# Kernel tuning notes

Hardware: AMD Instinct MI355X
Metric: run time of the kernel (lower is better)

Reference implementation:

```python
import jax, jax.numpy as jnp
import numpy as np

DIM = 128
DIM_HEAD = 32
HEADS = DIM // DIM_HEAD
WS = 7  # window_size
N = WS ** 3  # tokens per window = 343
TABLE = (2 * WS - 1) ** 3  # 2197


def _rel_pos_indices():
    pos = np.arange(WS)
    grid = np.stack(np.meshgrid(pos, pos, pos, indexing='ij'))  # [3,WS,WS,WS]
    grid = grid.reshape(3, -1).T  # [N,3]
    rel = grid[:, None, :] - grid[None, :, :] + (WS - 1)  # [N,N,3]
    idx = (rel * np.array([(2 * WS - 1) ** 2, 2 * WS - 1, 1])).sum(-1)
    return jnp.asarray(idx, jnp.int32)  # [N,N]


def setup_inputs() -> dict:
    key = jax.random.key(0)
    k1, k2, k3, k4 = jax.random.split(key, 4)
    x = jax.random.normal(k1, (2, 4, 4, 4, WS, WS, WS, DIM), dtype=jnp.float32)
    ln_w = jnp.ones((DIM,), jnp.float32)
    ln_b = jnp.zeros((DIM,), jnp.float32)
    w_qkv = jax.random.normal(k2, (DIM, 3 * DIM), jnp.float32) * 0.02
    w_out = jax.random.normal(k3, (DIM, DIM), jnp.float32) * 0.02
    bias_table = jax.random.normal(k4, (TABLE, HEADS), jnp.float32) * 0.02
    return {"x": x, "ln_w": ln_w, "ln_b": ln_b, "w_qkv": w_qkv,
            "w_out": w_out, "bias_table": bias_table,
            "rel_pos_indices": _rel_pos_indices()}


def reference(x, ln_w, ln_b, w_qkv, w_out, bias_table, rel_pos_indices):
    b, H, W, F, wh, ww, wf, d = x.shape
    scale = DIM_HEAD ** -0.5
    # LayerNorm over last dim (eps=1e-5, torch default)
    mu = x.mean(-1, keepdims=True)
    var = ((x - mu) ** 2).mean(-1, keepdims=True)
    xn = (x - mu) * jax.lax.rsqrt(var + 1e-5) * ln_w + ln_b
    # merge windows: [(b H W F), N, d]
    xr = xn.reshape(-1, wh * ww * wf, d)
    qkv = xr @ w_qkv  # [B, N, 3d]
    q, k, v = jnp.split(qkv, 3, axis=-1)
    def heads(t):
        B, n, _ = t.shape
        return t.reshape(B, n, HEADS, DIM_HEAD).transpose(0, 2, 1, 3)  # [B,h,N,dh]
    q, k, v = heads(q) * scale, heads(k), heads(v)
    sim = jnp.einsum('bhid,bhjd->bhij', q, k)  # [B,h,N,N]
    bias = bias_table[rel_pos_indices]  # [N,N,h]
    sim = sim + bias.transpose(2, 0, 1)[None]  # add [1,h,N,N]
    attn = jax.nn.softmax(sim, axis=-1)
    out = jnp.einsum('bhij,bhjd->bhid', attn, v)  # [B,h,N,dh]
    out = out.transpose(0, 2, 1, 3).reshape(-1, wh * ww * wf, d)
    out = out @ w_out
    return out.reshape(b, H, W, F, wh, ww, wf, d)
```

## Files before the change

### kernel.cpp

```cpp
#include <hip/hip_runtime.h>
#include <cstddef>
#include <cstdint>


#define NTOK 343
#define NPAD 352
#define NT   22
#define LOG2E 1.4426950408889634f
#define QSCALE (0.17677669529663687f * 1.4426950408889634f)

typedef short short8 __attribute__((ext_vector_type(8)));
typedef float f32x4  __attribute__((ext_vector_type(4)));

__device__ __forceinline__ unsigned short f2b(float f) {
    unsigned int u = __float_as_uint(f);
    u = (u + 0x7FFFu + ((u >> 16) & 1u)) >> 16;
    return (unsigned short)u;
}
__device__ __forceinline__ unsigned pk_bf16(float a, float b) {
    unsigned r;
    asm("v_cvt_pk_bf16_f32 %0, %1, %2" : "=v"(r) : "v"(a), "v"(b));
    return r;
}
__device__ __forceinline__ float fast_exp2(float x) {
#if __has_builtin(__builtin_amdgcn_exp2f)
    return __builtin_amdgcn_exp2f(x);
#else
    return exp2f(x);
#endif
}
__device__ __forceinline__ float blo(unsigned u){ return __uint_as_float(u << 16); }
__device__ __forceinline__ float bhi(unsigned u){ return __uint_as_float(u & 0xffff0000u); }

__global__ __launch_bounds__(256) void prep_weights(
    const float* __restrict__ wqkv, const float* __restrict__ wout,
    unsigned short* __restrict__ wqT_sw, unsigned short* __restrict__ woT)
{
    int t = blockIdx.x * 256 + threadIdx.x;
    if (t < 49152) {
        int s = t >> 14, within = t & 16383;
        int r = within & 127, k = within >> 7;
        float f = wqkv[k * 384 + s * 128 + r];
        if (s == 0) f *= QSCALE;
        wqT_sw[s * 16384 + ((r * 128 + k) ^ ((r & 7) << 3))] = f2b(f);
    } else {
        int t2 = t - 49152;
        int n = t2 & 127, k = t2 >> 7;
        woT[n * 128 + k] = f2b(wout[k * 128 + n]);
    }
}

__global__ __launch_bounds__(256) void prep_bias(
    const float* __restrict__ table, const int* __restrict__ rel,
    unsigned short* __restrict__ biasb)
{
    int t = blockIdx.x * 256 + threadIdx.x;
    int r  = t & 3;
    int tp = (t >> 2) & 1;
    int i  = (t >> 3) % NPAD;
    int rest = (t >> 3) / NPAD;
    int g  = rest & 3;  rest >>= 2;
    int c  = rest % 11;
    int h  = rest / 11;
    int j  = (2 * c + tp) * 16 + g * 4 + r;
    float v;
    if (j >= NTOK)      v = -1e30f;
    else if (i >= NTOK) v = 0.0f;
    else                v = table[rel[i * NTOK + j] * 4 + h] * LOG2E;
    biasb[t] = f2b(v);
}

__global__ __launch_bounds__(256) void ln_x(
    const float* __restrict__ x, const float* __restrict__ lnw, const float* __restrict__ lnb,
    unsigned short* __restrict__ xnsw)
{
    const int by = blockIdx.x, t = threadIdx.x;
    const int r = t >> 1, hf = t & 1;
    const size_t row = (size_t)by * 128 + r;
    const float* src = x + row * 128 + hf * 64;
    char* dst = reinterpret_cast<char*>(xnsw) + (size_t)by * 32768;
    float vals[64];
    float s = 0.f, s2 = 0.f;
    #pragma unroll
    for (int c = 0; c < 16; ++c) {
        float4 v = *reinterpret_cast<const float4*>(src + c * 4);
        vals[c*4+0] = v.x; vals[c*4+1] = v.y; vals[c*4+2] = v.z; vals[c*4+3] = v.w;
        s  += v.x + v.y + v.z + v.w;
        s2 += v.x*v.x + v.y*v.y + v.z*v.z + v.w*v.w;
    }
    s  += __shfl_xor(s, 1, 64);
    s2 += __shfl_xor(s2, 1, 64);
    const float mu   = s * (1.f / 128.f);
    const float var  = s2 * (1.f / 128.f) - mu * mu;
    const float rstd = rsqrtf(var + 1e-5f);
    #pragma unroll
    for (int c = 0; c < 8; ++c) {
        unsigned int packed[4];
        #pragma unroll
        for (int e = 0; e < 4; ++e) {
            int idx = c * 8 + e * 2;
            int col = hf * 64 + idx;
            float a = (vals[idx]   - mu) * rstd * lnw[col]   + lnb[col];
            float b = (vals[idx+1] - mu) * rstd * lnw[col+1] + lnb[col+1];
            packed[e] = pk_bf16(a, b);
        }
        int off = (r * 256 + hf * 128 + c * 16) ^ ((r & 7) << 4);
        *reinterpret_cast<int4*>(dst + off) = *reinterpret_cast<const int4*>(packed);
    }
}

__global__ __launch_bounds__(256) void qkv_gemm(
    const unsigned short* __restrict__ xnsw, const unsigned short* __restrict__ wqT_sw,
    unsigned short* __restrict__ qkv_rm)
{
    __shared__ __align__(16) char smem[65536];
    const int bx = blockIdx.x, by = blockIdx.y, t = threadIdx.x;

    {
        const char* srcA = reinterpret_cast<const char*>(xnsw) + (size_t)by * 32768;
        const char* srcB = reinterpret_cast<const char*>(wqT_sw) + (size_t)bx * 32768;
        #pragma unroll
        for (int p = 0; p < 8; ++p) {
            int off = p * 4096 + t * 16;
            *reinterpret_cast<int4*>(smem + off) = *reinterpret_cast<const int4*>(srcA + off);
            *reinterpret_cast<int4*>(smem + 32768 + off) = *reinterpret_cast<const int4*>(srcB + off);
        }
    }
    __syncthreads();

    const int lane = t & 63, wid = t >> 6;
    const int l15 = lane & 15, g = lane >> 4;
    const int wr = wid >> 1, wc = wid & 1;

    f32x4 acc[4][4] = {};
    #pragma unroll
    for (int ks = 0; ks < 4; ++ks) {
        short8 a[4], b[4];
        #pragma unroll
        for (int mt = 0; mt < 4; ++mt) {
            int row = wr * 64 + mt * 16 + l15;
            int off = (row * 256 + ks * 64 + g * 16) ^ ((row & 7) << 4);
            a[mt] = *reinterpret_cast<const short8*>(smem + off);
        }
        #pragma unroll
        for (int nt = 0; nt < 4; ++nt) {
            int row = wc * 64 + nt * 16 + l15;
            int off = (row * 256 + ks * 64 + g * 16) ^ ((row & 7) << 4);
            b[nt] = *reinterpret_cast<const short8*>(smem + 32768 + off);
        }
        #pragma unroll
        for (int mt = 0; mt < 4; ++mt)
            #pragma unroll
            for (int nt = 0; nt < 4; ++nt)
                acc[mt][nt] = __builtin_amdgcn_mfma_f32_16x16x32_bf16(a[mt], b[nt], acc[mt][nt], 0, 0, 0);
    }
    __syncthreads();

    #pragma unroll
    for (int mt = 0; mt < 4; ++mt) {
        #pragma unroll
        for (int nt = 0; nt < 4; ++nt) {
            unsigned w01 = pk_bf16(acc[mt][nt][0], acc[mt][nt][1]);
            unsigned w23 = pk_bf16(acc[mt][nt][2], acc[mt][nt][3]);
            int col = wc * 64 + nt * 16 + l15;
            int rb  = wr * 64 + mt * 16 + g * 4;
            unsigned short v4[4] = {(unsigned short)w01, (unsigned short)(w01 >> 16),
                                    (unsigned short)w23, (unsigned short)(w23 >> 16)};
            #pragma unroll
            for (int r4 = 0; r4 < 4; ++r4) {
                int row = rb + r4;
                int off = (row * 256 + col * 2) ^ ((row & 28) << 2);
                *reinterpret_cast<unsigned short*>(smem + off) = v4[r4];
            }
        }
    }
    __syncthreads();

    #pragma unroll
    for (int p = 0; p < 8; ++p) {
        int flat = p * 4096 + t * 16;
        int row = flat >> 8, cb = flat & 255;
        int off = (row * 256 + cb) ^ ((row & 28) << 2);
        int4 v = *reinterpret_cast<const int4*>(smem + off);
        unsigned token = (unsigned)(by * 128 + row);
        unsigned w = token / 343u;
        unsigned n = token - w * 343u;
        *reinterpret_cast<int4*>(qkv_rm + ((size_t)w * NPAD + n) * 384 + bx * 128 + (cb >> 1)) = v;
    }
}

__global__ __launch_bounds__(512, 4) void attn(
    const unsigned short* __restrict__ qkv_rm, const unsigned short* __restrict__ biasb,
    unsigned short* __restrict__ ao)
{
    __shared__ __align__(16) unsigned short klds[4 * NPAD * 8];
    __shared__ __align__(16) unsigned short vlds[44 * 272];
    __shared__ __align__(16) unsigned short pbuf[8][4][16][8];
    const int bw = blockIdx.x >> 2, h = blockIdx.x & 3;
    const int t = threadIdx.x, lane = t & 63, wid = t >> 6;
    const int l15 = lane & 15, g = lane >> 4;

    const unsigned short* base = qkv_rm + (size_t)bw * NPAD * 384;

    #pragma unroll
    for (int p = 0; p < 6; ++p) {
        int id = p * 512 + t;
        if (id < 2816) {
            bool isK = id < 1408;
            int id2 = isK ? id : id - 1408;
            int n = id2 >> 2, q4 = id2 & 3;
            const unsigned short* src = base + (size_t)n * 384 + (isK ? 128 : 256) + h * 32 + q4 * 8;
            int4 v = *reinterpret_cast<const int4*>(src);
            if (isK) {
                *reinterpret_cast<int4*>(&klds[(q4 * NPAD + n) * 8]) = v;
            } else {
                const unsigned short* sv = reinterpret_cast<const unsigned short*>(&v);
                int jb = n >> 3, e = n & 7;
                #pragma unroll
                for (int q = 0; q < 8; ++q)
                    vlds[jb * 272 + (q4 * 8 + q) * 8 + e] = sv[q];
            }
        }
    }
    __syncthreads();

    const f32x4 zero4 = {0.f, 0.f, 0.f, 0.f};
    for (int it = wid; it < NT; it += 8) {
        const int i = it * 16 + l15;
        short8 qf = *reinterpret_cast<const short8*>(base + (size_t)i * 384 + h * 32 + g * 8);
        short8 bb[11];
        #pragma unroll
        for (int c = 0; c < 11; ++c)
            bb[c] = *reinterpret_cast<const short8*>(biasb + (size_t)(((h * 11 + c) * 4 + g) * NPAD + i) * 8);

        float s = 0.f;
        f32x4 o0 = zero4, o1 = zero4;
        #pragma unroll
        for (int c = 0; c < 11; ++c) {
            short8 kf0 = *reinterpret_cast<const short8*>(&klds[(g * NPAD + 2 * c * 16 + l15) * 8]);
            short8 kf1 = *reinterpret_cast<const short8*>(&klds[(g * NPAD + (2 * c + 1) * 16 + l15) * 8]);
            f32x4 a0 = __builtin_amdgcn_mfma_f32_16x16x32_bf16(kf0, qf, zero4, 0, 0, 0);
            f32x4 a1 = __builtin_amdgcn_mfma_f32_16x16x32_bf16(kf1, qf, zero4, 0, 0, 0);
            const unsigned* bu = reinterpret_cast<const unsigned*>(&bb[c]);
            float p0 = fast_exp2(a0[0] + blo(bu[0]));
            float p1 = fast_exp2(a0[1] + bhi(bu[0]));
            float p2 = fast_exp2(a0[2] + blo(bu[1]));
            float p3 = fast_exp2(a0[3] + bhi(bu[1]));
            float p4 = fast_exp2(a1[0] + blo(bu[2]));
            float p5 = fast_exp2(a1[1] + bhi(bu[2]));
            float p6 = fast_exp2(a1[2] + blo(bu[3]));
            float p7 = fast_exp2(a1[3] + bhi(bu[3]));
            s += ((p0 + p1) + (p2 + p3)) + ((p4 + p5) + (p6 + p7));
            uint2 w0; w0.x = pk_bf16(p0, p1); w0.y = pk_bf16(p2, p3);
            uint2 w1; w1.x = pk_bf16(p4, p5); w1.y = pk_bf16(p6, p7);
            *reinterpret_cast<uint2*>(&pbuf[wid][(g >> 1)][l15][(g & 1) * 4]) = w0;
            *reinterpret_cast<uint2*>(&pbuf[wid][2 + (g >> 1)][l15][(g & 1) * 4]) = w1;
            short8 pf = *reinterpret_cast<const short8*>(&pbuf[wid][g][l15][0]);
            short8 vf0 = *reinterpret_cast<const short8*>(&vlds[(c * 4 + g) * 272 + l15 * 8]);
            short8 vf1 = *reinterpret_cast<const short8*>(&vlds[(c * 4 + g) * 272 + (16 + l15) * 8]);
            o0 = __builtin_amdgcn_mfma_f32_16x16x32_bf16(vf0, pf, o0, 0, 0, 0);
            o1 = __builtin_amdgcn_mfma_f32_16x16x32_bf16(vf1, pf, o1, 0, 0, 0);
        }
        s += __shfl_xor(s, 16, 64);
        s += __shfl_xor(s, 32, 64);
        const float rinv = 1.f / s;

        unsigned short* aorow = ao + ((size_t)bw * NPAD + i) * 128 + h * 32;
        uint2 q0; q0.x = pk_bf16(o0[0] * rinv, o0[1] * rinv); q0.y = pk_bf16(o0[2] * rinv, o0[3] * rinv);
        uint2 q1; q1.x = pk_bf16(o1[0] * rinv, o1[1] * rinv); q1.y = pk_bf16(o1[2] * rinv, o1[3] * rinv);
        *reinterpret_cast<uint2*>(aorow + g * 4) = q0;
        *reinterpret_cast<uint2*>(aorow + 16 + g * 4) = q1;
    }
}

__global__ __launch_bounds__(256) void outproj(
    const unsigned short* __restrict__ ao, const unsigned short* __restrict__ woT,
    float* __restrict__ out)
{
    __shared__ __align__(16) char smem[65536];
    const int t = threadIdx.x;
    const int m0 = blockIdx.x * 128;
    {
        const int r = t >> 1, hf = t & 1;
        const unsigned short* src = ao + (size_t)(m0 + r) * 128 + hf * 64;
        #pragma unroll
        for (int c = 0; c < 8; ++c) {
            int4 v = *reinterpret_cast<const int4*>(src + c * 8);
            int off = (r * 256 + hf * 128 + c * 16) ^ ((r & 7) << 4);
            *reinterpret_cast<int4*>(smem + off) = v;
        }
        const unsigned short* src2 = woT + (size_t)r * 128 + hf * 64;
        #pragma unroll
        for (int c = 0; c < 8; ++c) {
            int4 v = *reinterpret_cast<const int4*>(src2 + c * 8);
            int off = (r * 256 + hf * 128 + c * 16) ^ ((r & 7) << 4);
            *reinterpret_cast<int4*>(smem + 32768 + off) = v;
        }
    }
    __syncthreads();

    const int lane = t & 63, wid = t >> 6;
    const int l15 = lane & 15, g = lane >> 4;
    const int wr = wid >> 1, wc = wid & 1;
    f32x4 acc[4][4] = {};
    #pragma unroll
    for (int ks = 0; ks < 4; ++ks) {
        short8 a[4], b[4];
        #pragma unroll
        for (int mt = 0; mt < 4; ++mt) {
            int row = wr * 64 + mt * 16 + l15;
            int off = (row * 256 + ks * 64 + g * 16) ^ ((row & 7) << 4);
            a[mt] = *reinterpret_cast<const short8*>(smem + off);
        }
        #pragma unroll
        for (int nt = 0; nt < 4; ++nt) {
            int row = wc * 64 + nt * 16 + l15;
            int off = (row * 256 + ks * 64 + g * 16) ^ ((row & 7) << 4);
            b[nt] = *reinterpret_cast<const short8*>(smem + 32768 + off);
        }
        #pragma unroll
        for (int mt = 0; mt < 4; ++mt)
            #pragma unroll
            for (int nt = 0; nt < 4; ++nt)
                acc[mt][nt] = __builtin_amdgcn_mfma_f32_16x16x32_bf16(a[mt], b[nt], acc[mt][nt], 0, 0, 0);
    }
    #pragma unroll
    for (int mt = 0; mt < 4; ++mt) {
        #pragma unroll
        for (int r4 = 0; r4 < 4; ++r4) {
            int row = wr * 64 + mt * 16 + g * 4 + r4;
            unsigned R = (unsigned)(m0 + row);
            unsigned w = R / 352u;
            unsigned n = R - w * 352u;
            if (n < NTOK) {
                float* orow = out + ((size_t)w * NTOK + n) * 128;
                #pragma unroll
                for (int nt = 0; nt < 4; ++nt)
                    orow[wc * 64 + nt * 16 + l15] = acc[mt][nt][r4];
            }
        }
    }
}

extern "C" void kernel_launch(void* const* d_in, const int* in_sizes, int n_in,
                              void* d_out, int out_size, void* d_ws, size_t ws_size,
                              hipStream_t stream)
{
    const float* x     = (const float*)d_in[0];
    const float* lnw   = (const float*)d_in[1];
    const float* lnb   = (const float*)d_in[2];
    const float* wqkv  = (const float*)d_in[3];
    const float* wout  = (const float*)d_in[4];
    const float* table = (const float*)d_in[5];
    const int*   rel   = (const int*)d_in[6];
    float* out = (float*)d_out;

    char* ws = (char*)d_ws;
    unsigned short* qkv_rm = (unsigned short*)(ws + 0);
    unsigned short* ao     = (unsigned short*)(ws + 34603008);
    unsigned short* biasb  = (unsigned short*)(ws + 46137344);
    unsigned short* xnsw   = (unsigned short*)(ws + 47128576);
    unsigned short* wqT_sw = (unsigned short*)(ws + 58368000);
    unsigned short* woT    = (unsigned short*)(ws + 58466304);

    prep_weights<<<256, 256, 0, stream>>>(wqkv, wout, wqT_sw, woT);
    prep_bias<<<1936, 256, 0, stream>>>(table, rel, biasb);
    ln_x<<<343, 256, 0, stream>>>(x, lnw, lnb, xnsw);
    qkv_gemm<<<dim3(3, 343), 256, 0, stream>>>(xnsw, wqT_sw, qkv_rm);
    attn<<<512, 512, 0, stream>>>(qkv_rm, biasb, ao);
    outproj<<<352, 256, 0, stream>>>(ao, woT, out);
}
```

Measured before the change: 144.6 us.

## Merge prep kernels, software-pipeline attention PV, stage outproj stores through LDS

Merges the weight, bias and layernorm prep kernels into one launch dispatched by block index, removing two kernel launches. In the attention kernel the P buffer is double-buffered so each iteration's PV MFMAs consume the previous chunk's probabilities while the current QK scores are computed, hiding LDS write-read latency. The out-projection now writes its accumulators into swizzled LDS and then emits coalesced float4 stores instead of scattered scalar stores. The costs are more LDS, an extra barrier, and more branching in the merged prep kernel.

```diff
diff --git a/kernel.cpp b/kernel.cpp
--- a/kernel.cpp
+++ b/kernel.cpp
@@ -32,80 +32,76 @@
 __device__ __forceinline__ float blo(unsigned u){ return __uint_as_float(u << 16); }
 __device__ __forceinline__ float bhi(unsigned u){ return __uint_as_float(u & 0xffff0000u); }
 
-__global__ __launch_bounds__(256) void prep_weights(
+__global__ __launch_bounds__(256) void prep_all(
+    const float* __restrict__ x, const float* __restrict__ lnw, const float* __restrict__ lnb,
     const float* __restrict__ wqkv, const float* __restrict__ wout,
-    unsigned short* __restrict__ wqT_sw, unsigned short* __restrict__ woT)
+    const float* __restrict__ table, const int* __restrict__ rel,
+    unsigned short* __restrict__ wqT_sw, unsigned short* __restrict__ woT,
+    unsigned short* __restrict__ biasb, unsigned short* __restrict__ xnsw)
 {
-    int t = blockIdx.x * 256 + threadIdx.x;
-    if (t < 49152) {
-        int s = t >> 14, within = t & 16383;
-        int r = within & 127, k = within >> 7;
-        float f = wqkv[k * 384 + s * 128 + r];
-        if (s == 0) f *= QSCALE;
-        wqT_sw[s * 16384 + ((r * 128 + k) ^ ((r & 7) << 3))] = f2b(f);
+    const int b = blockIdx.x;
+    if (b < 256) {
+        int t = b * 256 + threadIdx.x;
+        if (t < 49152) {
+            int s = t >> 14, within = t & 16383;
+            int r = within & 127, k = within >> 7;
+            float f = wqkv[k * 384 + s * 128 + r];
+            if (s == 0) f *= QSCALE;
+            wqT_sw[s * 16384 + ((r * 128 + k) ^ ((r & 7) << 3))] = f2b(f);
+        } else {
+            int t2 = t - 49152;
+            int n = t2 & 127, k = t2 >> 7;
+            woT[n * 128 + k] = f2b(wout[k * 128 + n]);
+        }
+    } else if (b < 2192) {
+        int t = (b - 256) * 256 + threadIdx.x;
+        int r  = t & 3;
+        int tp = (t >> 2) & 1;
+        int i  = (t >> 3) % NPAD;
+        int rest = (t >> 3) / NPAD;
+        int g  = rest & 3;  rest >>= 2;
+        int c  = rest % 11;
+        int h  = rest / 11;
+        int j  = (2 * c + tp) * 16 + g * 4 + r;
+        float v;
+        if (j >= NTOK)      v = -1e30f;
+        else if (i >= NTOK) v = 0.0f;
+        else                v = table[rel[i * NTOK + j] * 4 + h] * LOG2E;
+        biasb[t] = f2b(v);
     } else {
-        int t2 = t - 49152;
-        int n = t2 & 127, k = t2 >> 7;
-        woT[n * 128 + k] = f2b(wout[k * 128 + n]);
-    }
-}
-
-__global__ __launch_bounds__(256) void prep_bias(
-    const float* __restrict__ table, const int* __restrict__ rel,
-    unsigned short* __restrict__ biasb)
-{
-    int t = blockIdx.x * 256 + threadIdx.x;
-    int r  = t & 3;
-    int tp = (t >> 2) & 1;
-    int i  = (t >> 3) % NPAD;
-    int rest = (t >> 3) / NPAD;
-    int g  = rest & 3;  rest >>= 2;
-    int c  = rest % 11;
-    int h  = rest / 11;
-    int j  = (2 * c + tp) * 16 + g * 4 + r;
-    float v;
-    if (j >= NTOK)      v = -1e30f;
-    else if (i >= NTOK) v = 0.0f;
-    else                v = table[rel[i * NTOK + j] * 4 + h] * LOG2E;
-    biasb[t] = f2b(v);
-}
-
-__global__ __launch_bounds__(256) void ln_x(
-    const float* __restrict__ x, const float* __restrict__ lnw, const float* __restrict__ lnb,
-    unsigned short* __restrict__ xnsw)
-{
-    const int by = blockIdx.x, t = threadIdx.x;
-    const int r = t >> 1, hf = t & 1;
-    const size_t row = (size_t)by * 128 + r;
-    const float* src = x + row * 128 + hf * 64;
-    char* dst = reinterpret_cast<char*>(xnsw) + (size_t)by * 32768;
-    float vals[64];
-    float s = 0.f, s2 = 0.f;
-    #pragma unroll
-    for (int c = 0; c < 16; ++c) {
-        float4 v = *reinterpret_cast<const float4*>(src + c * 4);
-        vals[c*4+0] = v.x; vals[c*4+1] = v.y; vals[c*4+2] = v.z; vals[c*4+3] = v.w;
-        s  += v.x + v.y + v.z + v.w;
-        s2 += v.x*v.x + v.y*v.y + v.z*v.z + v.w*v.w;
-    }
-    s  += __shfl_xor(s, 1, 64);
-    s2 += __shfl_xor(s2, 1, 64);
-    const float mu   = s * (1.f / 128.f);
-    const float var  = s2 * (1.f / 128.f) - mu * mu;
-    const float rstd = rsqrtf(var + 1e-5f);
-    #pragma unroll
-    for (int c = 0; c < 8; ++c) {
-        unsigned int packed[4];
-        #pragma unroll
-        for (int e = 0; e < 4; ++e) {
-            int idx = c * 8 + e * 2;
-            int col = hf * 64 + idx;
-            float a = (vals[idx]   - mu) * rstd * lnw[col]   + lnb[col];
-            float b = (vals[idx+1] - mu) * rstd * lnw[col+1] + lnb[col+1];
-            packed[e] = pk_bf16(a, b);
-        }
-        int off = (r * 256 + hf * 128 + c * 16) ^ ((r & 7) << 4);
-        *reinterpret_cast<int4*>(dst + off) = *reinterpret_cast<const int4*>(packed);
+        const int by = b - 2192, t = threadIdx.x;
+        const int r = t >> 1, hf = t & 1;
+        const size_t row = (size_t)by * 128 + r;
+        const float* src = x + row * 128 + hf * 64;
+        char* dst = reinterpret_cast<char*>(xnsw) + (size_t)by * 32768;
+        float vals[64];
+        float s = 0.f, s2 = 0.f;
+        #pragma unroll
+        for (int c = 0; c < 16; ++c) {
+            float4 v = *reinterpret_cast<const float4*>(src + c * 4);
+            vals[c*4+0] = v.x; vals[c*4+1] = v.y; vals[c*4+2] = v.z; vals[c*4+3] = v.w;
+            s  += v.x + v.y + v.z + v.w;
+            s2 += v.x*v.x + v.y*v.y + v.z*v.z + v.w*v.w;
+        }
+        s  += __shfl_xor(s, 1, 64);
+        s2 += __shfl_xor(s2, 1, 64);
+        const float mu   = s * (1.f / 128.f);
+        const float var  = s2 * (1.f / 128.f) - mu * mu;
+        const float rstd = rsqrtf(var + 1e-5f);
+        #pragma unroll
+        for (int c = 0; c < 8; ++c) {
+            unsigned int packed[4];
+            #pragma unroll
+            for (int e = 0; e < 4; ++e) {
+                int idx = c * 8 + e * 2;
+                int col = hf * 64 + idx;
+                float a2 = (vals[idx]   - mu) * rstd * lnw[col]   + lnb[col];
+                float b2 = (vals[idx+1] - mu) * rstd * lnw[col+1] + lnb[col+1];
+                packed[e] = pk_bf16(a2, b2);
+            }
+            int off = (r * 256 + hf * 128 + c * 16) ^ ((r & 7) << 4);
+            *reinterpret_cast<int4*>(dst + off) = *reinterpret_cast<const int4*>(packed);
+        }
     }
 }
 
@@ -195,7 +191,7 @@
 {
     __shared__ __align__(16) unsigned short klds[4 * NPAD * 8];
     __shared__ __align__(16) unsigned short vlds[44 * 272];
-    __shared__ __align__(16) unsigned short pbuf[8][4][16][8];
+    __shared__ __align__(16) unsigned short pbuf[8][2][4][16][8];
     const int bw = blockIdx.x >> 2, h = blockIdx.x & 3;
     const int t = threadIdx.x, lane = t & 63, wid = t >> 6;
     const int l15 = lane & 15, g = lane >> 4;
@@ -235,12 +231,41 @@
 
         float s = 0.f;
         f32x4 o0 = zero4, o1 = zero4;
-        #pragma unroll
-        for (int c = 0; c < 11; ++c) {
+
+        {
+            short8 kf0 = *reinterpret_cast<const short8*>(&klds[(g * NPAD + l15) * 8]);
+            short8 kf1 = *reinterpret_cast<const short8*>(&klds[(g * NPAD + 16 + l15) * 8]);
+            f32x4 a0 = __builtin_amdgcn_mfma_f32_16x16x32_bf16(kf0, qf, zero4, 0, 0, 0);
+            f32x4 a1 = __builtin_amdgcn_mfma_f32_16x16x32_bf16(kf1, qf, zero4, 0, 0, 0);
+            const unsigned* bu = reinterpret_cast<const unsigned*>(&bb[0]);
+            float p0 = fast_exp2(a0[0] + blo(bu[0]));
+            float p1 = fast_exp2(a0[1] + bhi(bu[0]));
+            float p2 = fast_exp2(a0[2] + blo(bu[1]));
+            float p3 = fast_exp2(a0[3] + bhi(bu[1]));
+            float p4 = fast_exp2(a1[0] + blo(bu[2]));
+            float p5 = fast_exp2(a1[1] + bhi(bu[2]));
+            float p6 = fast_exp2(a1[2] + blo(bu[3]));
+            float p7 = fast_exp2(a1[3] + bhi(bu[3]));
+            s += ((p0 + p1) + (p2 + p3)) + ((p4 + p5) + (p6 + p7));
+            uint2 w0; w0.x = pk_bf16(p0, p1); w0.y = pk_bf16(p2, p3);
+            uint2 w1; w1.x = pk_bf16(p4, p5); w1.y = pk_bf16(p6, p7);
+            *reinterpret_cast<uint2*>(&pbuf[wid][0][(g >> 1)][l15][(g & 1) * 4]) = w0;
+            *reinterpret_cast<uint2*>(&pbuf[wid][0][2 + (g >> 1)][l15][(g & 1) * 4]) = w1;
+        }
+
+        #pragma unroll
+        for (int c = 1; c < 11; ++c) {
             short8 kf0 = *reinterpret_cast<const short8*>(&klds[(g * NPAD + 2 * c * 16 + l15) * 8]);
             short8 kf1 = *reinterpret_cast<const short8*>(&klds[(g * NPAD + (2 * c + 1) * 16 + l15) * 8]);
             f32x4 a0 = __builtin_amdgcn_mfma_f32_16x16x32_bf16(kf0, qf, zero4, 0, 0, 0);
             f32x4 a1 = __builtin_amdgcn_mfma_f32_16x16x32_bf16(kf1, qf, zero4, 0, 0, 0);
+
+            short8 pf = *reinterpret_cast<const short8*>(&pbuf[wid][(c - 1) & 1][g][l15][0]);
+            short8 vf0 = *reinterpret_cast<const short8*>(&vlds[((c - 1) * 4 + g) * 272 + l15 * 8]);
+            short8 vf1 = *reinterpret_cast<const short8*>(&vlds[((c - 1) * 4 + g) * 272 + (16 + l15) * 8]);
+            o0 = __builtin_amdgcn_mfma_f32_16x16x32_bf16(vf0, pf, o0, 0, 0, 0);
+            o1 = __builtin_amdgcn_mfma_f32_16x16x32_bf16(vf1, pf, o1, 0, 0, 0);
+
             const unsigned* bu = reinterpret_cast<const unsigned*>(&bb[c]);
             float p0 = fast_exp2(a0[0] + blo(bu[0]));
             float p1 = fast_exp2(a0[1] + bhi(bu[0]));
@@ -253,14 +278,18 @@
             s += ((p0 + p1) + (p2 + p3)) + ((p4 + p5) + (p6 + p7));
             uint2 w0; w0.x = pk_bf16(p0, p1); w0.y = pk_bf16(p2, p3);
             uint2 w1; w1.x = pk_bf16(p4, p5); w1.y = pk_bf16(p6, p7);
-            *reinterpret_cast<uint2*>(&pbuf[wid][(g >> 1)][l15][(g & 1) * 4]) = w0;
-            *reinterpret_cast<uint2*>(&pbuf[wid][2 + (g >> 1)][l15][(g & 1) * 4]) = w1;
-            short8 pf = *reinterpret_cast<const short8*>(&pbuf[wid][g][l15][0]);
-            short8 vf0 = *reinterpret_cast<const short8*>(&vlds[(c * 4 + g) * 272 + l15 * 8]);
-            short8 vf1 = *reinterpret_cast<const short8*>(&vlds[(c * 4 + g) * 272 + (16 + l15) * 8]);
+            *reinterpret_cast<uint2*>(&pbuf[wid][c & 1][(g >> 1)][l15][(g & 1) * 4]) = w0;
+            *reinterpret_cast<uint2*>(&pbuf[wid][c & 1][2 + (g >> 1)][l15][(g & 1) * 4]) = w1;
+        }
+
+        {
+            short8 pf = *reinterpret_cast<const short8*>(&pbuf[wid][0][g][l15][0]);
+            short8 vf0 = *reinterpret_cast<const short8*>(&vlds[(10 * 4 + g) * 272 + l15 * 8]);
+            short8 vf1 = *reinterpret_cast<const short8*>(&vlds[(10 * 4 + g) * 272 + (16 + l15) * 8]);
             o0 = __builtin_amdgcn_mfma_f32_16x16x32_bf16(vf0, pf, o0, 0, 0, 0);
             o1 = __builtin_amdgcn_mfma_f32_16x16x32_bf16(vf1, pf, o1, 0, 0, 0);
         }
+
         s += __shfl_xor(s, 16, 64);
         s += __shfl_xor(s, 32, 64);
         const float rinv = 1.f / s;
@@ -324,21 +353,34 @@
             for (int nt = 0; nt < 4; ++nt)
                 acc[mt][nt] = __builtin_amdgcn_mfma_f32_16x16x32_bf16(a[mt], b[nt], acc[mt][nt], 0, 0, 0);
     }
+    __syncthreads();
+
     #pragma unroll
     for (int mt = 0; mt < 4; ++mt) {
         #pragma unroll
-        for (int r4 = 0; r4 < 4; ++r4) {
-            int row = wr * 64 + mt * 16 + g * 4 + r4;
-            unsigned R = (unsigned)(m0 + row);
-            unsigned w = R / 352u;
-            unsigned n = R - w * 352u;
-            if (n < NTOK) {
-                float* orow = out + ((size_t)w * NTOK + n) * 128;
-                #pragma unroll
-                for (int nt = 0; nt < 4; ++nt)
-                    orow[wc * 64 + nt * 16 + l15] = acc[mt][nt][r4];
+        for (int nt = 0; nt < 4; ++nt) {
+            int col = wc * 64 + nt * 16 + l15;
+            #pragma unroll
+            for (int r4 = 0; r4 < 4; ++r4) {
+                int row = wr * 64 + mt * 16 + g * 4 + r4;
+                int off = row * 512 + ((col * 4 + ((row >> 2) & 3) * 32) & 511);
+                *reinterpret_cast<float*>(smem + off) = acc[mt][nt][r4];
             }
         }
+    }
+    __syncthreads();
+
+    #pragma unroll
+    for (int p = 0; p < 16; ++p) {
+        int flat = p * 4096 + t * 16;
+        int row = flat >> 9, cbB = flat & 511;
+        int off = row * 512 + ((cbB + ((row >> 2) & 3) * 32) & 511);
+        float4 v = *reinterpret_cast<const float4*>(smem + off);
+        unsigned R = (unsigned)(m0 + row);
+        unsigned w = R / 352u;
+        unsigned n = R - w * 352u;
+        if (n < NTOK)
+            *reinterpret_cast<float4*>(out + ((size_t)w * NTOK + n) * 128 + (cbB >> 2)) = v;
     }
 }
 
@@ -363,9 +405,8 @@
     unsigned short* wqT_sw = (unsigned short*)(ws + 58368000);
     unsigned short* woT    = (unsigned short*)(ws + 58466304);
 
-    prep_weights<<<256, 256, 0, stream>>>(wqkv, wout, wqT_sw, woT);
-    prep_bias<<<1936, 256, 0, stream>>>(table, rel, biasb);
-    ln_x<<<343, 256, 0, stream>>>(x, lnw, lnb, xnsw);
+    prep_all<<<2535, 256, 0, stream>>>(x, lnw, lnb, wqkv, wout, table, rel,
+                                       wqT_sw, woT, biasb, xnsw);
     qkv_gemm<<<dim3(3, 343), 256, 0, stream>>>(xnsw, wqT_sw, qkv_rm);
     attn<<<512, 512, 0, stream>>>(qkv_rm, biasb, ao);
     outproj<<<352, 256, 0, stream>>>(ao, woT, out);
```

Measured after the change: 146.5 us. Within noise of the previous version (+1.3%).
